# Kernel tuning notes

Measured on AMD Instinct MI355X. Metric: run time of the kernel, lower is better.

The kernel has to match this reference:

```python
import jax, jax.numpy as jnp
import numpy as np

N_HEADS = 8
N_LANDMARKS = 64
NEWTON_ITERS = 6


def _iterative_inv(mat):
    # mat: [B,H,L,L]; Newton-Schulz approximate inverse, 6 iterations
    L = mat.shape[-1]
    fro = jnp.sqrt(jnp.sum(mat * mat, axis=(-2, -1), keepdims=True))
    fro = jnp.maximum(fro, 1e-6)
    z = jnp.swapaxes(mat, -2, -1) / (fro * fro)
    for _ in range(NEWTON_ITERS):
        z = 2.0 * z - z @ mat @ z
    return z


def setup_inputs() -> dict:
    key = jax.random.key(0)
    ks = jax.random.split(key, 5)
    B, N, C = 4, 8192, 512
    s = 1.0 / np.sqrt(C)
    return {
        "x": jax.random.normal(ks[0], (B, N, C), jnp.float32),
        "Wqkv": jax.random.normal(ks[1], (3 * C, C), jnp.float32) * s,
        "bqkv": jax.random.normal(ks[2], (3 * C,), jnp.float32) * 0.01,
        "Wproj": jax.random.normal(ks[3], (C, C), jnp.float32) * s,
        "bproj": jax.random.normal(ks[4], (C,), jnp.float32) * 0.01,
    }


def reference(x, Wqkv, bqkv, Wproj, bproj):
    B, N, C = x.shape
    H = N_HEADS
    hd = C // H
    scale = hd ** (-0.5)
    n_lm = N_LANDMARKS

    qkv = x @ Wqkv.T + bqkv                       # [B,N,3C]
    qkv = qkv.reshape(B, N, 3, H, hd).transpose(2, 0, 3, 1, 4)  # [3,B,H,N,hd]
    q, k, v = qkv[0], qkv[1], qkv[2]

    if N <= n_lm:
        attn = jax.nn.softmax(q @ jnp.swapaxes(k, -2, -1) * scale, axis=-1)
        out = attn @ v
    else:
        stride = max(N // n_lm, 1)
        lm_idx = jnp.arange(0, N, stride)[:n_lm]
        q_lm = q[:, :, lm_idx]                    # [B,H,L,hd]
        k_lm = k[:, :, lm_idx]
        kernel_1 = jax.nn.softmax(q @ jnp.swapaxes(k_lm, -2, -1) * scale, axis=-1)   # [B,H,N,L]
        kernel_2 = jax.nn.softmax(q_lm @ jnp.swapaxes(k_lm, -2, -1) * scale, axis=-1)  # [B,H,L,L]
        kernel_3 = jax.nn.softmax(q_lm @ jnp.swapaxes(k, -2, -1) * scale, axis=-1)   # [B,H,L,N]
        kernel_2_inv = _iterative_inv(kernel_2)
        out = kernel_1 @ (kernel_2_inv @ (kernel_3 @ v))  # [B,H,N,hd]

    out = jnp.swapaxes(out, 1, 2).reshape(B, N, C)
    return out @ Wproj.T + bproj
```

## Files before the change

### kernel.cpp

```cpp
#include <hip/hip_runtime.h>

typedef unsigned short u16;
typedef unsigned int u32;

typedef __bf16 v8bf __attribute__((ext_vector_type(8)));
typedef float v4f __attribute__((ext_vector_type(4)));
typedef u16 v8u __attribute__((ext_vector_type(8)));

#define N_TOK 8192
#define CDIM 512
#define HEADS 8
#define HD 64
#define LM 64
#define LSTRIDE 128
#define BHN 32
#define NCHUNK 32
#define CHUNK 256
#define SCALE 0.125f

__device__ __forceinline__ float b2f(u16 u) { return __uint_as_float(((u32)u) << 16); }
__device__ __forceinline__ u16 f2bf(float f) {
  u32 u = __float_as_uint(f);
  u += 0x7fffu + ((u >> 16) & 1u);
  return (u16)(u >> 16);
}
__device__ __forceinline__ u32 pk2bf(float a, float b) {
  return (u32)f2bf(a) | ((u32)f2bf(b) << 16);
}

__device__ __forceinline__ void gl_lds16(const u16* g, u16* l) {
  __builtin_amdgcn_global_load_lds(
      (const __attribute__((address_space(1))) u32*)g,
      (__attribute__((address_space(3))) u32*)l, 16, 0, 0);
}

__device__ __forceinline__ void wr_hl(u16* __restrict__ h, u16* __restrict__ l,
                                      int row, int col, float v) {
  u16 hi = f2bf(v);
  u16 lo = f2bf(v - b2f(hi));
  int a = row * 64 + (((col >> 3) ^ (row & 7)) << 3) + (col & 7);
  h[a] = hi;
  l[a] = lo;
}

__global__ __launch_bounds__(256) void cast_bf16(const float* __restrict__ src,
                                                 u16* __restrict__ dst, int n8) {
  int i = blockIdx.x * 256 + threadIdx.x;
  if (i >= n8) return;
  const float4* s = (const float4*)src;
  float4 a = s[(size_t)i * 2], b = s[(size_t)i * 2 + 1];
  uint4 o;
  o.x = (u32)f2bf(a.x) | ((u32)f2bf(a.y) << 16);
  o.y = (u32)f2bf(a.z) | ((u32)f2bf(a.w) << 16);
  o.z = (u32)f2bf(b.x) | ((u32)f2bf(b.y) << 16);
  o.w = (u32)f2bf(b.z) | ((u32)f2bf(b.w) << 16);
  *(uint4*)(dst + (size_t)i * 8) = o;
}

__global__ __launch_bounds__(256) void cast_w2(const float* __restrict__ wa,
                                               const float* __restrict__ wb,
                                               u16* __restrict__ da,
                                               u16* __restrict__ db) {
  int i = blockIdx.x * 256 + threadIdx.x;
  const float* src;
  u16* dst;
  int j;
  if (i < 98304) { src = wa; dst = da; j = i; }
  else           { src = wb; dst = db; j = i - 98304; }
  const float4* s = (const float4*)src;
  float4 a = s[(size_t)j * 2], b = s[(size_t)j * 2 + 1];
  uint4 o;
  o.x = (u32)f2bf(a.x) | ((u32)f2bf(a.y) << 16);
  o.y = (u32)f2bf(a.z) | ((u32)f2bf(a.w) << 16);
  o.z = (u32)f2bf(b.x) | ((u32)f2bf(b.y) << 16);
  o.w = (u32)f2bf(b.z) | ((u32)f2bf(b.w) << 16);
  *(uint4*)(dst + (size_t)j * 8) = o;
}

template <int MODE>
__global__ __launch_bounds__(256) void gemm_bt(const u16* __restrict__ A,
                                               const u16* __restrict__ Bm,
                                               const float* __restrict__ bias,
                                               u16* __restrict__ qo,
                                               u16* __restrict__ ko,
                                               u16* __restrict__ vo,
                                               float* __restrict__ outp) {
  __shared__ __align__(16) u16 As[128 * 32];
  __shared__ __align__(16) u16 Bs[128 * 32];
  const int K = 512;
  const int m0 = blockIdx.x * 128;
  const int n0 = blockIdx.y * 128;
  const int t = threadIdx.x;
  const int lane = t & 63, w = t >> 6;
  const int wm = w >> 1, wn = w & 1;
  const int quad = lane >> 4, lrow = lane & 15;

  v4f acc[4][4];
#pragma unroll
  for (int i = 0; i < 4; ++i)
#pragma unroll
    for (int j = 0; j < 4; ++j)
#pragma unroll
      for (int r = 0; r < 4; ++r) acc[i][j][r] = 0.f;

  for (int kt = 0; kt < K; kt += 32) {
    __syncthreads();
#pragma unroll
    for (int p = 0; p < 2; ++p) {
      int ci = p * 256 + t;
      int r = ci >> 2, s = ci & 3;
      int cs = (s ^ (r >> 1)) & 3;
      gl_lds16(A + (size_t)(m0 + r) * K + kt + cs * 8, &As[ci * 8]);
      gl_lds16(Bm + (size_t)(n0 + r) * K + kt + cs * 8, &Bs[ci * 8]);
    }
    __syncthreads();
    v8bf af[4], bf[4];
#pragma unroll
    for (int ti = 0; ti < 4; ++ti) {
      int row = wm * 64 + ti * 16 + lrow;
      af[ti] = *(const v8bf*)&As[row * 32 + ((quad ^ (row >> 1)) & 3) * 8];
    }
#pragma unroll
    for (int tj = 0; tj < 4; ++tj) {
      int row = wn * 64 + tj * 16 + lrow;
      bf[tj] = *(const v8bf*)&Bs[row * 32 + ((quad ^ (row >> 1)) & 3) * 8];
    }
#pragma unroll
    for (int ti = 0; ti < 4; ++ti)
#pragma unroll
      for (int tj = 0; tj < 4; ++tj)
        acc[ti][tj] = __builtin_amdgcn_mfma_f32_16x16x32_bf16(af[ti], bf[tj], acc[ti][tj], 0, 0, 0);
  }

#pragma unroll
  for (int ti = 0; ti < 4; ++ti) {
#pragma unroll
    for (int tj = 0; tj < 4; ++tj) {
      int gn = n0 + wn * 64 + tj * 16 + lrow;
      float bv = bias[gn];
#pragma unroll
      for (int r = 0; r < 4; ++r) {
        int gm = m0 + wm * 64 + ti * 16 + quad * 4 + r;
        float val = acc[ti][tj][r] + bv;
        if (MODE == 0) {
          int tt = gn >> 9;
          int h = (gn >> 6) & 7;
          int d = gn & 63;
          int b = gm >> 13;
          int n = gm & 8191;
          size_t di = ((size_t)(b * HEADS + h) * N_TOK + n) * HD + d;
          u16* dst = (tt == 0) ? qo : (tt == 1) ? ko : vo;
          dst[di] = f2bf(val);
        } else {
          outp[(size_t)gm * CDIM + gn] = val;
        }
      }
    }
  }
}

__global__ __launch_bounds__(256) void fpart(const u16* __restrict__ qb,
                                             const u16* __restrict__ kb,
                                             const u16* __restrict__ vb,
                                             float* __restrict__ Fp,
                                             float* __restrict__ Mc,
                                             float* __restrict__ Sc) {
  __shared__ __align__(16) char smem[4 * 64 * 40 * 2 * 2];
  __shared__ float msh[4][64], ssh[4][64];
  const int jc = blockIdx.x, bh = blockIdx.y;
  const int t = threadIdx.x;
  const int lane = t & 63, w = t >> 6;
  const int col = lane & 15, quad = lane >> 4;
  const int jq = lane & 7, dh = lane >> 3;

  u16* Pw = (u16*)smem + w * (64 * 40);
  u16* vT = (u16*)smem + 4 * (64 * 40) + w * (64 * 40);
  float* Fbuf = (float*)smem;

  v8bf qf[4][2];
#pragma unroll
  for (int it = 0; it < 4; ++it)
#pragma unroll
    for (int kh = 0; kh < 2; ++kh)
      qf[it][kh] = *(const v8bf*)(qb + ((size_t)bh * N_TOK + (size_t)(it * 16 + col) * LSTRIDE) * HD + kh * 32 + quad * 8);

  float mw[4], sw[4];
  v4f facc[4][4];
#pragma unroll
  for (int it = 0; it < 4; ++it) { mw[it] = -3.0e38f; sw[it] = 0.f; }
#pragma unroll
  for (int dt = 0; dt < 4; ++dt)
#pragma unroll
    for (int it = 0; it < 4; ++it)
#pragma unroll
      for (int r = 0; r < 4; ++r) facc[dt][it][r] = 0.f;

  const size_t kv0 = (size_t)bh * N_TOK + jc * CHUNK + w * 64;

  v8bf kf[2][2];
  v8u vr[4];
#pragma unroll
  for (int jt = 0; jt < 2; ++jt)
#pragma unroll
    for (int kh = 0; kh < 2; ++kh)
      kf[jt][kh] = *(const v8bf*)(kb + (kv0 + jt * 16 + col) * HD + kh * 32 + quad * 8);
#pragma unroll
  for (int e = 0; e < 4; ++e)
    vr[e] = *(const v8u*)(vb + (kv0 + jq * 4 + e) * HD + dh * 8);

#pragma unroll
  for (int st = 0; st < 2; ++st) {
#pragma unroll
    for (int e = 0; e < 8; ++e) {
      uint2 pk;
      pk.x = (u32)vr[0][e] | ((u32)vr[1][e] << 16);
      pk.y = (u32)vr[2][e] | ((u32)vr[3][e] << 16);
      *(uint2*)&vT[(dh * 8 + e) * 40 + jq * 4] = pk;
    }

    v8bf kfn[2][2];
    v8u vrn[4];
    if (st < 1) {
      const size_t bn = kv0 + 32;
#pragma unroll
      for (int jt = 0; jt < 2; ++jt)
#pragma unroll
        for (int kh = 0; kh < 2; ++kh)
          kfn[jt][kh] = *(const v8bf*)(kb + (bn + jt * 16 + col) * HD + kh * 32 + quad * 8);
    }

    v4f sacc[2][4];
#pragma unroll
    for (int jt = 0; jt < 2; ++jt)
#pragma unroll
      for (int it = 0; it < 4; ++it) {
#pragma unroll
        for (int r = 0; r < 4; ++r) sacc[jt][it][r] = 0.f;
#pragma unroll
        for (int kh = 0; kh < 2; ++kh)
          sacc[jt][it] = __builtin_amdgcn_mfma_f32_16x16x32_bf16(kf[jt][kh], qf[it][kh], sacc[jt][it], 0, 0, 0);
      }

    if (st < 1) {
      const size_t bn = kv0 + 32;
#pragma unroll
      for (int e = 0; e < 4; ++e)
        vrn[e] = *(const v8u*)(vb + (bn + jq * 4 + e) * HD + dh * 8);
    }

#pragma unroll
    for (int it = 0; it < 4; ++it) {
      float mloc = -3.0e38f;
#pragma unroll
      for (int jt = 0; jt < 2; ++jt)
#pragma unroll
        for (int r = 0; r < 4; ++r) {
          float s = sacc[jt][it][r] * SCALE;
          sacc[jt][it][r] = s;
          mloc = fmaxf(mloc, s);
        }
      mloc = fmaxf(mloc, __shfl_xor(mloc, 16));
      mloc = fmaxf(mloc, __shfl_xor(mloc, 32));
      float mnew = fmaxf(mw[it], mloc);
      float alpha = __expf(mw[it] - mnew);
      mw[it] = mnew;
      float rs = 0.f;
#pragma unroll
      for (int jt = 0; jt < 2; ++jt)
#pragma unroll
        for (int r = 0; r < 4; ++r) {
          float p = __expf(sacc[jt][it][r] - mnew);
          sacc[jt][it][r] = p;
          rs += p;
        }
      rs += __shfl_xor(rs, 16);
      rs += __shfl_xor(rs, 32);
      sw[it] = sw[it] * alpha + rs;
#pragma unroll
      for (int jt = 0; jt < 2; ++jt) {
        uint2 pk;
        pk.x = pk2bf(sacc[jt][it][0], sacc[jt][it][1]);
        pk.y = pk2bf(sacc[jt][it][2], sacc[jt][it][3]);
        *(uint2*)&Pw[(it * 16 + col) * 40 + jt * 16 + quad * 4] = pk;
      }
#pragma unroll
      for (int dt = 0; dt < 4; ++dt)
#pragma unroll
        for (int r = 0; r < 4; ++r) facc[dt][it][r] *= alpha;
    }

    v8bf vfr[4], pfr[4];
#pragma unroll
    for (int dt = 0; dt < 4; ++dt)
      vfr[dt] = *(const v8bf*)&vT[(dt * 16 + col) * 40 + quad * 8];
#pragma unroll
    for (int it = 0; it < 4; ++it)
      pfr[it] = *(const v8bf*)&Pw[(it * 16 + col) * 40 + quad * 8];
#pragma unroll
    for (int dt = 0; dt < 4; ++dt)
#pragma unroll
      for (int it = 0; it < 4; ++it)
        facc[dt][it] = __builtin_amdgcn_mfma_f32_16x16x32_bf16(vfr[dt], pfr[it], facc[dt][it], 0, 0, 0);

    if (st < 1) {
#pragma unroll
      for (int jt = 0; jt < 2; ++jt)
#pragma unroll
        for (int kh = 0; kh < 2; ++kh)
          kf[jt][kh] = kfn[jt][kh];
#pragma unroll
      for (int e = 0; e < 4; ++e) vr[e] = vrn[e];
    }
  }

  if (quad == 0) {
#pragma unroll
    for (int it = 0; it < 4; ++it) {
      msh[w][it * 16 + col] = mw[it];
      ssh[w][it * 16 + col] = sw[it];
    }
  }
  __syncthreads();

  const size_t cb = (size_t)(bh * NCHUNK + jc) * 64;
  float scl[4];
#pragma unroll
  for (int it = 0; it < 4; ++it) {
    int i = it * 16 + col;
    float m0 = msh[0][i], m1 = msh[1][i], m2 = msh[2][i], m3 = msh[3][i];
    float M = fmaxf(fmaxf(m0, m1), fmaxf(m2, m3));
    float e0 = __expf(m0 - M), e1 = __expf(m1 - M);
    float e2 = __expf(m2 - M), e3 = __expf(m3 - M);
    float Stot = e0 * ssh[0][i] + e1 * ssh[1][i] + e2 * ssh[2][i] + e3 * ssh[3][i];
    scl[it] = (w == 0) ? e0 : (w == 1) ? e1 : (w == 2) ? e2 : e3;
    if (w == 0 && quad == 0) {
      Mc[cb + i] = M;
      Sc[cb + i] = Stot;
    }
  }

  for (int wv = 0; wv < 4; ++wv) {
    if (w == wv) {
#pragma unroll
      for (int it = 0; it < 4; ++it)
#pragma unroll
        for (int dt = 0; dt < 4; ++dt) {
          float* dst = &Fbuf[(it * 16 + col) * 76 + dt * 16 + quad * 4];
          float4 v;
          v.x = facc[dt][it][0] * scl[it];
          v.y = facc[dt][it][1] * scl[it];
          v.z = facc[dt][it][2] * scl[it];
          v.w = facc[dt][it][3] * scl[it];
          if (wv == 0) {
            *(float4*)dst = v;
          } else {
            float4 o = *(float4*)dst;
            o.x += v.x; o.y += v.y; o.z += v.z; o.w += v.w;
            *(float4*)dst = o;
          }
        }
    }
    __syncthreads();
  }

  size_t base = (size_t)(bh * NCHUNK + jc) * 4096;
#pragma unroll
  for (int p = 0; p < 16; ++p) {
    int idx = p * 256 + t;
    Fp[base + idx] = Fbuf[(idx >> 6) * 76 + (idx & 63)];
  }
}

__device__ __forceinline__ void mm_hl(const u16* __restrict__ Ah,
                                      const u16* __restrict__ Al,
                                      const u16* __restrict__ Bh,
                                      const u16* __restrict__ Bl,
                                      int Ra, int quad, int lrow, v4f out[4]) {
  v8bf ah[2], al[2];
#pragma unroll
  for (int kk = 0; kk < 2; ++kk) {
    int c8 = (((kk * 4 + quad) ^ (Ra & 7)) * 8);
    ah[kk] = *(const v8bf*)&Ah[Ra * 64 + c8];
    al[kk] = *(const v8bf*)&Al[Ra * 64 + c8];
  }
#pragma unroll
  for (int nt = 0; nt < 4; ++nt) {
    int Rb = nt * 16 + lrow;
#pragma unroll
    for (int kk = 0; kk < 2; ++kk) {
      int c8 = (((kk * 4 + quad) ^ (Rb & 7)) * 8);
      v8bf bh = *(const v8bf*)&Bh[Rb * 64 + c8];
      v8bf bl = *(const v8bf*)&Bl[Rb * 64 + c8];
      out[nt] = __builtin_amdgcn_mfma_f32_16x16x32_bf16(ah[kk], bh, out[nt], 0, 0, 0);
      out[nt] = __builtin_amdgcn_mfma_f32_16x16x32_bf16(ah[kk], bl, out[nt], 0, 0, 0);
      out[nt] = __builtin_amdgcn_mfma_f32_16x16x32_bf16(al[kk], bh, out[nt], 0, 0, 0);
    }
  }
}

__global__ __launch_bounds__(256) void newton_t(const u16* __restrict__ qb,
                                                const u16* __restrict__ kb,
                                                const float* __restrict__ Fp,
                                                const float* __restrict__ Mc,
                                                const float* __restrict__ Sc,
                                                u16* __restrict__ Tt) {
  __shared__ float Sf[4096];
  __shared__ float red[4];
  __shared__ __align__(16) u16 mTh[4096], mTl[4096];
  __shared__ __align__(16) u16 zh_[4096], zl_[4096];
  __shared__ __align__(16) u16 zTh[4096], zTl[4096];
  __shared__ __align__(16) u16 wh_[4096], wl_[4096];
  const int bh = blockIdx.x;
  const int t = threadIdx.x, lane = t & 63, w = t >> 6;
  const int quad = lane >> 4, lrow = lane & 15;
  const int Ra = w * 16 + lrow;
  const int Rd = w * 16 + quad * 4;

  {
    v8bf qf[2], kf[4][2];
#pragma unroll
    for (int kk = 0; kk < 2; ++kk)
      qf[kk] = *(const v8bf*)(qb + ((size_t)bh * N_TOK + (size_t)Ra * LSTRIDE) * HD + kk * 32 + quad * 8);
#pragma unroll
    for (int nt = 0; nt < 4; ++nt)
#pragma unroll
      for (int kk = 0; kk < 2; ++kk)
        kf[nt][kk] = *(const v8bf*)(kb + ((size_t)bh * N_TOK + (size_t)(nt * 16 + lrow) * LSTRIDE) * HD + kk * 32 + quad * 8);
    v4f sa[4];
#pragma unroll
    for (int nt = 0; nt < 4; ++nt) {
#pragma unroll
      for (int r = 0; r < 4; ++r) sa[nt][r] = 0.f;
#pragma unroll
      for (int kk = 0; kk < 2; ++kk)
        sa[nt] = __builtin_amdgcn_mfma_f32_16x16x32_bf16(qf[kk], kf[nt][kk], sa[nt], 0, 0, 0);
    }
#pragma unroll
    for (int nt = 0; nt < 4; ++nt)
#pragma unroll
      for (int r = 0; r < 4; ++r)
        Sf[(Rd + r) * 64 + nt * 16 + lrow] = sa[nt][r] * SCALE;
  }
  __syncthreads();

  for (int rr = 0; rr < 16; ++rr) {
    int i = w * 16 + rr;
    float vv = Sf[i * 64 + lane];
    float m = vv;
#pragma unroll
    for (int off = 32; off; off >>= 1) m = fmaxf(m, __shfl_xor(m, off));
    float e = expf(vv - m);
    float s = e;
#pragma unroll
    for (int off = 32; off; off >>= 1) s += __shfl_xor(s, off);
    Sf[i * 64 + lane] = e / s;
  }
  __syncthreads();

  float loc = 0.f;
#pragma unroll
  for (int p = 0; p < 16; ++p) {
    float v = Sf[p * 256 + t];
    loc += v * v;
  }
#pragma unroll
  for (int off = 32; off; off >>= 1) loc += __shfl_xor(loc, off);
  if (lane == 0) red[w] = loc;
  __syncthreads();
  float fro = fmaxf(sqrtf(red[0] + red[1] + red[2] + red[3]), 1e-6f);
  float inv = 1.0f / (fro * fro);

  for (int p = 0; p < 16; ++p) {
    int idx = p * 256 + t;
    int r = idx >> 6, c = idx & 63;
    float Mrc = Sf[r * 64 + c];
    float Mcr = Sf[c * 64 + r];
    wr_hl(mTh, mTl, r, c, Mcr);
    wr_hl(zh_, zl_, r, c, Mcr * inv);
    wr_hl(zTh, zTl, r, c, Mrc * inv);
  }
  float zr[4][4];
#pragma unroll
  for (int nt = 0; nt < 4; ++nt)
#pragma unroll
    for (int r = 0; r < 4; ++r)
      zr[nt][r] = Sf[(nt * 16 + lrow) * 64 + Rd + r] * inv;
  __syncthreads();

  for (int it = 0; it < 6; ++it) {
    v4f aw[4];
#pragma unroll
    for (int nt = 0; nt < 4; ++nt)
#pragma unroll
      for (int r = 0; r < 4; ++r) aw[nt][r] = 0.f;
    mm_hl(zh_, zl_, mTh, mTl, Ra, quad, lrow, aw);
#pragma unroll
    for (int nt = 0; nt < 4; ++nt)
#pragma unroll
      for (int r = 0; r < 4; ++r)
        wr_hl(wh_, wl_, Rd + r, nt * 16 + lrow, aw[nt][r]);
    __syncthreads();

    v4f ap[4];
#pragma unroll
    for (int nt = 0; nt < 4; ++nt)
#pragma unroll
      for (int r = 0; r < 4; ++r) ap[nt][r] = 0.f;
    mm_hl(wh_, wl_, zTh, zTl, Ra, quad, lrow, ap);
    float znr[4][4];
#pragma unroll
    for (int nt = 0; nt < 4; ++nt)
#pragma unroll
      for (int r = 0; r < 4; ++r)
        znr[nt][r] = 2.f * zr[nt][r] - ap[nt][r];
    __syncthreads();

#pragma unroll
    for (int nt = 0; nt < 4; ++nt)
#pragma unroll
      for (int r = 0; r < 4; ++r) {
        zr[nt][r] = znr[nt][r];
        wr_hl(zh_, zl_, Rd + r, nt * 16 + lrow, znr[nt][r]);
        wr_hl(zTh, zTl, nt * 16 + lrow, Rd + r, znr[nt][r]);
      }
    __syncthreads();
  }

  if (t < 64) {
    float M = -3.0e38f;
#pragma unroll
    for (int jc = 0; jc < NCHUNK; ++jc)
      M = fmaxf(M, Mc[(bh * NCHUNK + jc) * 64 + t]);
    float S = 0.f;
#pragma unroll
    for (int jc = 0; jc < NCHUNK; ++jc)
      S += expf(Mc[(bh * NCHUNK + jc) * 64 + t] - M) * Sc[(bh * NCHUNK + jc) * 64 + t];
    float invS = 1.0f / S;
#pragma unroll
    for (int jc = 0; jc < NCHUNK; ++jc)
      Sf[jc * 64 + t] = expf(Mc[(bh * NCHUNK + jc) * 64 + t] - M) * invS;
  }
  __syncthreads();

  for (int p = 0; p < 16; ++p) {
    int idx = p * 256 + t;
    int i = idx >> 6, d = idx & 63;
    float sum = 0.f;
#pragma unroll
    for (int jc = 0; jc < NCHUNK; ++jc)
      sum += Sf[jc * 64 + i] * Fp[(size_t)(bh * NCHUNK + jc) * 4096 + idx];
    wr_hl(wh_, wl_, d, i, sum);
  }
  __syncthreads();

  v4f at[4];
#pragma unroll
  for (int nt = 0; nt < 4; ++nt)
#pragma unroll
    for (int r = 0; r < 4; ++r) at[nt][r] = 0.f;
  mm_hl(zh_, zl_, wh_, wl_, Ra, quad, lrow, at);
#pragma unroll
  for (int nt = 0; nt < 4; ++nt)
#pragma unroll
    for (int r = 0; r < 4; ++r)
      Tt[(size_t)bh * 4096 + (size_t)(nt * 16 + lrow) * 64 + (Rd + r)] = f2bf(at[nt][r]);
}

__global__ __launch_bounds__(256) void attn_out_k(const u16* __restrict__ qb,
                                                  const u16* __restrict__ kb,
                                                  const u16* __restrict__ Tt,
                                                  u16* __restrict__ ao) {
  __shared__ __align__(16) u16 Pl[4][1024];
  const int bh = blockIdx.y;
  const int b = bh >> 3, h = bh & 7;
  const int t = threadIdx.x;
  const int lane = t & 63, w = t >> 6;
  const int col = lane & 15, quad = lane >> 4;
  const int rot = (col & 7) * 8;

  v8bf kfr[4][2], tfr[4][2];
#pragma unroll
  for (int tj = 0; tj < 4; ++tj)
#pragma unroll
    for (int kh = 0; kh < 2; ++kh)
      kfr[tj][kh] = *(const v8bf*)(kb + ((size_t)bh * N_TOK + (size_t)(tj * 16 + col) * LSTRIDE) * HD + kh * 32 + quad * 8);
#pragma unroll
  for (int td = 0; td < 4; ++td)
#pragma unroll
    for (int jh = 0; jh < 2; ++jh)
      tfr[td][jh] = *(const v8bf*)(Tt + (size_t)bh * 4096 + (size_t)(td * 16 + col) * 64 + jh * 32 + quad * 8);

  u16* Pw = &Pl[w][0];

  for (int tile = 0; tile < 4; ++tile) {
    const int n0 = blockIdx.x * 256 + w * 64 + tile * 16;
    v8bf qf[2];
#pragma unroll
    for (int kh = 0; kh < 2; ++kh)
      qf[kh] = *(const v8bf*)(qb + ((size_t)bh * N_TOK + n0 + col) * HD + kh * 32 + quad * 8);

    v4f S[4];
#pragma unroll
    for (int tj = 0; tj < 4; ++tj) {
#pragma unroll
      for (int r = 0; r < 4; ++r) S[tj][r] = 0.f;
#pragma unroll
      for (int kh = 0; kh < 2; ++kh)
        S[tj] = __builtin_amdgcn_mfma_f32_16x16x32_bf16(kfr[tj][kh], qf[kh], S[tj], 0, 0, 0);
    }

    float mx = -3.0e38f;
#pragma unroll
    for (int tj = 0; tj < 4; ++tj)
#pragma unroll
      for (int r = 0; r < 4; ++r) {
        S[tj][r] *= SCALE;
        mx = fmaxf(mx, S[tj][r]);
      }
    mx = fmaxf(mx, __shfl_xor(mx, 16));
    mx = fmaxf(mx, __shfl_xor(mx, 32));
    float sum = 0.f;
#pragma unroll
    for (int tj = 0; tj < 4; ++tj)
#pragma unroll
      for (int r = 0; r < 4; ++r) {
        S[tj][r] = __expf(S[tj][r] - mx);
        sum += S[tj][r];
      }
    sum += __shfl_xor(sum, 16);
    sum += __shfl_xor(sum, 32);
    float inv = 1.0f / sum;

#pragma unroll
    for (int tj = 0; tj < 4; ++tj) {
      u32 lo = (u32)f2bf(S[tj][0] * inv) | ((u32)f2bf(S[tj][1] * inv) << 16);
      u32 hi = (u32)f2bf(S[tj][2] * inv) | ((u32)f2bf(S[tj][3] * inv) << 16);
      uint2 pk = {lo, hi};
      *(uint2*)&Pw[col * 64 + ((tj * 16 + quad * 4 + rot) & 63)] = pk;
    }
    v8bf pf[2];
#pragma unroll
    for (int jh = 0; jh < 2; ++jh)
      pf[jh] = *(const v8bf*)&Pw[col * 64 + ((jh * 32 + quad * 8 + rot) & 63)];

    v4f O[4];
#pragma unroll
    for (int td = 0; td < 4; ++td) {
#pragma unroll
      for (int r = 0; r < 4; ++r) O[td][r] = 0.f;
#pragma unroll
      for (int jh = 0; jh < 2; ++jh)
        O[td] = __builtin_amdgcn_mfma_f32_16x16x32_bf16(pf[jh], tfr[td][jh], O[td], 0, 0, 0);
    }
#pragma unroll
    for (int td = 0; td < 4; ++td)
#pragma unroll
      for (int r = 0; r < 4; ++r) {
        int n = n0 + quad * 4 + r;
        ao[((size_t)(b * N_TOK + n)) * CDIM + h * HD + td * 16 + col] = f2bf(O[td][r]);
      }
  }
}

__global__ void ws_too_small_sentinel(float* out) {
  if (threadIdx.x == 0 && blockIdx.x == 0) out[0] = 1.0f;
}

static constexpr size_t SZ_QKV = (size_t)BHN * N_TOK * HD * 2;
static constexpr size_t OFF_Q = 0;
static constexpr size_t OFF_K = OFF_Q + SZ_QKV;
static constexpr size_t OFF_V = OFF_K + SZ_QKV;
static constexpr size_t OFF_FP = OFF_V + SZ_QKV;
static constexpr size_t SZ_FP = (size_t)BHN * NCHUNK * 4096 * 4;
static constexpr size_t OFF_MC = OFF_FP + SZ_FP;
static constexpr size_t SZ_MS = (size_t)BHN * NCHUNK * 64 * 4;
static constexpr size_t OFF_SC = OFF_MC + SZ_MS;
static constexpr size_t OFF_T = OFF_SC + SZ_MS;
static constexpr size_t OFF_WQ = OFF_T + (size_t)BHN * 4096 * 2;
static constexpr size_t OFF_WP = OFF_WQ + (size_t)3 * CDIM * CDIM * 2;
static constexpr size_t OFF_END = OFF_WP + (size_t)CDIM * CDIM * 2;

extern "C" void kernel_launch(void* const* d_in, const int* in_sizes, int n_in,
                              void* d_out, int out_size, void* d_ws, size_t ws_size,
                              hipStream_t stream) {
  const float* x = (const float*)d_in[0];
  const float* Wqkv = (const float*)d_in[1];
  const float* bqkv = (const float*)d_in[2];
  const float* Wproj = (const float*)d_in[3];
  const float* bproj = (const float*)d_in[4];
  float* out = (float*)d_out;
  char* ws = (char*)d_ws;
  if (ws_size < OFF_END) {
    ws_too_small_sentinel<<<1, 64, 0, stream>>>(out);
    return;
  }

  u16* qb = (u16*)(ws + OFF_Q);
  u16* kb = (u16*)(ws + OFF_K);
  u16* vb = (u16*)(ws + OFF_V);
  float* Fp = (float*)(ws + OFF_FP);
  float* Mc = (float*)(ws + OFF_MC);
  float* Sc = (float*)(ws + OFF_SC);
  u16* Tt = (u16*)(ws + OFF_T);
  u16* Wqb = (u16*)(ws + OFF_WQ);
  u16* Wpb = (u16*)(ws + OFF_WP);
  u16* attn = (u16*)(ws + OFF_V);
  u16* xb = (u16*)d_out;

  cast_bf16<<<8192, 256, 0, stream>>>(x, xb, 2097152);
  cast_w2<<<512, 256, 0, stream>>>(Wqkv, Wproj, Wqb, Wpb);
  gemm_bt<0><<<dim3(256, 12), 256, 0, stream>>>(xb, Wqb, bqkv, qb, kb, vb, nullptr);
  fpart<<<dim3(NCHUNK, BHN), 256, 0, stream>>>(qb, kb, vb, Fp, Mc, Sc);
  newton_t<<<dim3(BHN), 256, 0, stream>>>(qb, kb, Fp, Mc, Sc, Tt);
  attn_out_k<<<dim3(32, BHN), 256, 0, stream>>>(qb, kb, Tt, attn);
  gemm_bt<1><<<dim3(256, 4), 256, 0, stream>>>(attn, Wpb, bproj, nullptr, nullptr, nullptr, out);
}
```

Baseline: 302.8 us.

## Overlap Newton-Schulz inverse with partial K/V reduction in one launch

```diff
diff --git a/kernel.cpp b/kernel.cpp
--- a/kernel.cpp
+++ b/kernel.cpp
@@ -159,218 +159,6 @@
   }
 }
 
-__global__ __launch_bounds__(256) void fpart(const u16* __restrict__ qb,
-                                             const u16* __restrict__ kb,
-                                             const u16* __restrict__ vb,
-                                             float* __restrict__ Fp,
-                                             float* __restrict__ Mc,
-                                             float* __restrict__ Sc) {
-  __shared__ __align__(16) char smem[4 * 64 * 40 * 2 * 2];
-  __shared__ float msh[4][64], ssh[4][64];
-  const int jc = blockIdx.x, bh = blockIdx.y;
-  const int t = threadIdx.x;
-  const int lane = t & 63, w = t >> 6;
-  const int col = lane & 15, quad = lane >> 4;
-  const int jq = lane & 7, dh = lane >> 3;
-
-  u16* Pw = (u16*)smem + w * (64 * 40);
-  u16* vT = (u16*)smem + 4 * (64 * 40) + w * (64 * 40);
-  float* Fbuf = (float*)smem;
-
-  v8bf qf[4][2];
-#pragma unroll
-  for (int it = 0; it < 4; ++it)
-#pragma unroll
-    for (int kh = 0; kh < 2; ++kh)
-      qf[it][kh] = *(const v8bf*)(qb + ((size_t)bh * N_TOK + (size_t)(it * 16 + col) * LSTRIDE) * HD + kh * 32 + quad * 8);
-
-  float mw[4], sw[4];
-  v4f facc[4][4];
-#pragma unroll
-  for (int it = 0; it < 4; ++it) { mw[it] = -3.0e38f; sw[it] = 0.f; }
-#pragma unroll
-  for (int dt = 0; dt < 4; ++dt)
-#pragma unroll
-    for (int it = 0; it < 4; ++it)
-#pragma unroll
-      for (int r = 0; r < 4; ++r) facc[dt][it][r] = 0.f;
-
-  const size_t kv0 = (size_t)bh * N_TOK + jc * CHUNK + w * 64;
-
-  v8bf kf[2][2];
-  v8u vr[4];
-#pragma unroll
-  for (int jt = 0; jt < 2; ++jt)
-#pragma unroll
-    for (int kh = 0; kh < 2; ++kh)
-      kf[jt][kh] = *(const v8bf*)(kb + (kv0 + jt * 16 + col) * HD + kh * 32 + quad * 8);
-#pragma unroll
-  for (int e = 0; e < 4; ++e)
-    vr[e] = *(const v8u*)(vb + (kv0 + jq * 4 + e) * HD + dh * 8);
-
-#pragma unroll
-  for (int st = 0; st < 2; ++st) {
-#pragma unroll
-    for (int e = 0; e < 8; ++e) {
-      uint2 pk;
-      pk.x = (u32)vr[0][e] | ((u32)vr[1][e] << 16);
-      pk.y = (u32)vr[2][e] | ((u32)vr[3][e] << 16);
-      *(uint2*)&vT[(dh * 8 + e) * 40 + jq * 4] = pk;
-    }
-
-    v8bf kfn[2][2];
-    v8u vrn[4];
-    if (st < 1) {
-      const size_t bn = kv0 + 32;
-#pragma unroll
-      for (int jt = 0; jt < 2; ++jt)
-#pragma unroll
-        for (int kh = 0; kh < 2; ++kh)
-          kfn[jt][kh] = *(const v8bf*)(kb + (bn + jt * 16 + col) * HD + kh * 32 + quad * 8);
-    }
-
-    v4f sacc[2][4];
-#pragma unroll
-    for (int jt = 0; jt < 2; ++jt)
-#pragma unroll
-      for (int it = 0; it < 4; ++it) {
-#pragma unroll
-        for (int r = 0; r < 4; ++r) sacc[jt][it][r] = 0.f;
-#pragma unroll
-        for (int kh = 0; kh < 2; ++kh)
-          sacc[jt][it] = __builtin_amdgcn_mfma_f32_16x16x32_bf16(kf[jt][kh], qf[it][kh], sacc[jt][it], 0, 0, 0);
-      }
-
-    if (st < 1) {
-      const size_t bn = kv0 + 32;
-#pragma unroll
-      for (int e = 0; e < 4; ++e)
-        vrn[e] = *(const v8u*)(vb + (bn + jq * 4 + e) * HD + dh * 8);
-    }
-
-#pragma unroll
-    for (int it = 0; it < 4; ++it) {
-      float mloc = -3.0e38f;
-#pragma unroll
-      for (int jt = 0; jt < 2; ++jt)
-#pragma unroll
-        for (int r = 0; r < 4; ++r) {
-          float s = sacc[jt][it][r] * SCALE;
-          sacc[jt][it][r] = s;
-          mloc = fmaxf(mloc, s);
-        }
-      mloc = fmaxf(mloc, __shfl_xor(mloc, 16));
-      mloc = fmaxf(mloc, __shfl_xor(mloc, 32));
-      float mnew = fmaxf(mw[it], mloc);
-      float alpha = __expf(mw[it] - mnew);
-      mw[it] = mnew;
-      float rs = 0.f;
-#pragma unroll
-      for (int jt = 0; jt < 2; ++jt)
-#pragma unroll
-        for (int r = 0; r < 4; ++r) {
-          float p = __expf(sacc[jt][it][r] - mnew);
-          sacc[jt][it][r] = p;
-          rs += p;
-        }
-      rs += __shfl_xor(rs, 16);
-      rs += __shfl_xor(rs, 32);
-      sw[it] = sw[it] * alpha + rs;
-#pragma unroll
-      for (int jt = 0; jt < 2; ++jt) {
-        uint2 pk;
-        pk.x = pk2bf(sacc[jt][it][0], sacc[jt][it][1]);
-        pk.y = pk2bf(sacc[jt][it][2], sacc[jt][it][3]);
-        *(uint2*)&Pw[(it * 16 + col) * 40 + jt * 16 + quad * 4] = pk;
-      }
-#pragma unroll
-      for (int dt = 0; dt < 4; ++dt)
-#pragma unroll
-        for (int r = 0; r < 4; ++r) facc[dt][it][r] *= alpha;
-    }
-
-    v8bf vfr[4], pfr[4];
-#pragma unroll
-    for (int dt = 0; dt < 4; ++dt)
-      vfr[dt] = *(const v8bf*)&vT[(dt * 16 + col) * 40 + quad * 8];
-#pragma unroll
-    for (int it = 0; it < 4; ++it)
-      pfr[it] = *(const v8bf*)&Pw[(it * 16 + col) * 40 + quad * 8];
-#pragma unroll
-    for (int dt = 0; dt < 4; ++dt)
-#pragma unroll
-      for (int it = 0; it < 4; ++it)
-        facc[dt][it] = __builtin_amdgcn_mfma_f32_16x16x32_bf16(vfr[dt], pfr[it], facc[dt][it], 0, 0, 0);
-
-    if (st < 1) {
-#pragma unroll
-      for (int jt = 0; jt < 2; ++jt)
-#pragma unroll
-        for (int kh = 0; kh < 2; ++kh)
-          kf[jt][kh] = kfn[jt][kh];
-#pragma unroll
-      for (int e = 0; e < 4; ++e) vr[e] = vrn[e];
-    }
-  }
-
-  if (quad == 0) {
-#pragma unroll
-    for (int it = 0; it < 4; ++it) {
-      msh[w][it * 16 + col] = mw[it];
-      ssh[w][it * 16 + col] = sw[it];
-    }
-  }
-  __syncthreads();
-
-  const size_t cb = (size_t)(bh * NCHUNK + jc) * 64;
-  float scl[4];
-#pragma unroll
-  for (int it = 0; it < 4; ++it) {
-    int i = it * 16 + col;
-    float m0 = msh[0][i], m1 = msh[1][i], m2 = msh[2][i], m3 = msh[3][i];
-    float M = fmaxf(fmaxf(m0, m1), fmaxf(m2, m3));
-    float e0 = __expf(m0 - M), e1 = __expf(m1 - M);
-    float e2 = __expf(m2 - M), e3 = __expf(m3 - M);
-    float Stot = e0 * ssh[0][i] + e1 * ssh[1][i] + e2 * ssh[2][i] + e3 * ssh[3][i];
-    scl[it] = (w == 0) ? e0 : (w == 1) ? e1 : (w == 2) ? e2 : e3;
-    if (w == 0 && quad == 0) {
-      Mc[cb + i] = M;
-      Sc[cb + i] = Stot;
-    }
-  }
-
-  for (int wv = 0; wv < 4; ++wv) {
-    if (w == wv) {
-#pragma unroll
-      for (int it = 0; it < 4; ++it)
-#pragma unroll
-        for (int dt = 0; dt < 4; ++dt) {
-          float* dst = &Fbuf[(it * 16 + col) * 76 + dt * 16 + quad * 4];
-          float4 v;
-          v.x = facc[dt][it][0] * scl[it];
-          v.y = facc[dt][it][1] * scl[it];
-          v.z = facc[dt][it][2] * scl[it];
-          v.w = facc[dt][it][3] * scl[it];
-          if (wv == 0) {
-            *(float4*)dst = v;
-          } else {
-            float4 o = *(float4*)dst;
-            o.x += v.x; o.y += v.y; o.z += v.z; o.w += v.w;
-            *(float4*)dst = o;
-          }
-        }
-    }
-    __syncthreads();
-  }
-
-  size_t base = (size_t)(bh * NCHUNK + jc) * 4096;
-#pragma unroll
-  for (int p = 0; p < 16; ++p) {
-    int idx = p * 256 + t;
-    Fp[base + idx] = Fbuf[(idx >> 6) * 76 + (idx & 63)];
-  }
-}
-
 __device__ __forceinline__ void mm_hl(const u16* __restrict__ Ah,
                                       const u16* __restrict__ Al,
                                       const u16* __restrict__ Bh,
@@ -398,17 +186,360 @@
   }
 }
 
-__global__ __launch_bounds__(256) void newton_t(const u16* __restrict__ qb,
+__global__ __launch_bounds__(256) void fpart_nz(const u16* __restrict__ qb,
                                                 const u16* __restrict__ kb,
-                                                const float* __restrict__ Fp,
-                                                const float* __restrict__ Mc,
-                                                const float* __restrict__ Sc,
-                                                u16* __restrict__ Tt) {
-  __shared__ float Sf[4096];
+                                                const u16* __restrict__ vb,
+                                                float* __restrict__ Fp,
+                                                float* __restrict__ Mc,
+                                                float* __restrict__ Sc,
+                                                u16* __restrict__ Zb) {
+  __shared__ __align__(16) char smem[65536];
+  __shared__ float msh[4][64], ssh[4][64];
   __shared__ float red[4];
-  __shared__ __align__(16) u16 mTh[4096], mTl[4096];
+  const int jc = blockIdx.x, bh = blockIdx.y;
+  const int t = threadIdx.x;
+  const int lane = t & 63, w = t >> 6;
+  const int col = lane & 15, quad = lane >> 4;
+
+  if (jc < NCHUNK) {
+    const int jq = lane & 7, dh = lane >> 3;
+    u16* Pw = (u16*)smem + w * (64 * 40);
+    u16* vT = (u16*)smem + 4 * (64 * 40) + w * (64 * 40);
+    float* Fbuf = (float*)smem;
+
+    v8bf qf[4][2];
+#pragma unroll
+    for (int it = 0; it < 4; ++it)
+#pragma unroll
+      for (int kh = 0; kh < 2; ++kh)
+        qf[it][kh] = *(const v8bf*)(qb + ((size_t)bh * N_TOK + (size_t)(it * 16 + col) * LSTRIDE) * HD + kh * 32 + quad * 8);
+
+    float mw[4], sw[4];
+    v4f facc[4][4];
+#pragma unroll
+    for (int it = 0; it < 4; ++it) { mw[it] = -3.0e38f; sw[it] = 0.f; }
+#pragma unroll
+    for (int dt = 0; dt < 4; ++dt)
+#pragma unroll
+      for (int it = 0; it < 4; ++it)
+#pragma unroll
+        for (int r = 0; r < 4; ++r) facc[dt][it][r] = 0.f;
+
+    const size_t kv0 = (size_t)bh * N_TOK + jc * CHUNK + w * 64;
+
+    v8bf kf[2][2];
+    v8u vr[4];
+#pragma unroll
+    for (int jt = 0; jt < 2; ++jt)
+#pragma unroll
+      for (int kh = 0; kh < 2; ++kh)
+        kf[jt][kh] = *(const v8bf*)(kb + (kv0 + jt * 16 + col) * HD + kh * 32 + quad * 8);
+#pragma unroll
+    for (int e = 0; e < 4; ++e)
+      vr[e] = *(const v8u*)(vb + (kv0 + jq * 4 + e) * HD + dh * 8);
+
+#pragma unroll
+    for (int st = 0; st < 2; ++st) {
+#pragma unroll
+      for (int e = 0; e < 8; ++e) {
+        uint2 pk;
+        pk.x = (u32)vr[0][e] | ((u32)vr[1][e] << 16);
+        pk.y = (u32)vr[2][e] | ((u32)vr[3][e] << 16);
+        *(uint2*)&vT[(dh * 8 + e) * 40 + jq * 4] = pk;
+      }
+
+      v8bf kfn[2][2];
+      v8u vrn[4];
+      if (st < 1) {
+        const size_t bn = kv0 + 32;
+#pragma unroll
+        for (int jt = 0; jt < 2; ++jt)
+#pragma unroll
+          for (int kh = 0; kh < 2; ++kh)
+            kfn[jt][kh] = *(const v8bf*)(kb + (bn + jt * 16 + col) * HD + kh * 32 + quad * 8);
+      }
+
+      v4f sacc[2][4];
+#pragma unroll
+      for (int jt = 0; jt < 2; ++jt)
+#pragma unroll
+        for (int it = 0; it < 4; ++it) {
+#pragma unroll
+          for (int r = 0; r < 4; ++r) sacc[jt][it][r] = 0.f;
+#pragma unroll
+          for (int kh = 0; kh < 2; ++kh)
+            sacc[jt][it] = __builtin_amdgcn_mfma_f32_16x16x32_bf16(kf[jt][kh], qf[it][kh], sacc[jt][it], 0, 0, 0);
+        }
+
+      if (st < 1) {
+        const size_t bn = kv0 + 32;
+#pragma unroll
+        for (int e = 0; e < 4; ++e)
+          vrn[e] = *(const v8u*)(vb + (bn + jq * 4 + e) * HD + dh * 8);
+      }
+
+#pragma unroll
+      for (int it = 0; it < 4; ++it) {
+        float mloc = -3.0e38f;
+#pragma unroll
+        for (int jt = 0; jt < 2; ++jt)
+#pragma unroll
+          for (int r = 0; r < 4; ++r) {
+            float s = sacc[jt][it][r] * SCALE;
+            sacc[jt][it][r] = s;
+            mloc = fmaxf(mloc, s);
+          }
+        mloc = fmaxf(mloc, __shfl_xor(mloc, 16));
+        mloc = fmaxf(mloc, __shfl_xor(mloc, 32));
+        float mnew = fmaxf(mw[it], mloc);
+        float alpha = __expf(mw[it] - mnew);
+        mw[it] = mnew;
+        float rs = 0.f;
+#pragma unroll
+        for (int jt = 0; jt < 2; ++jt)
+#pragma unroll
+          for (int r = 0; r < 4; ++r) {
+            float p = __expf(sacc[jt][it][r] - mnew);
+            sacc[jt][it][r] = p;
+            rs += p;
+          }
+        rs += __shfl_xor(rs, 16);
+        rs += __shfl_xor(rs, 32);
+        sw[it] = sw[it] * alpha + rs;
+#pragma unroll
+        for (int jt = 0; jt < 2; ++jt) {
+          uint2 pk;
+          pk.x = pk2bf(sacc[jt][it][0], sacc[jt][it][1]);
+          pk.y = pk2bf(sacc[jt][it][2], sacc[jt][it][3]);
+          *(uint2*)&Pw[(it * 16 + col) * 40 + jt * 16 + quad * 4] = pk;
+        }
+#pragma unroll
+        for (int dt = 0; dt < 4; ++dt)
+#pragma unroll
+          for (int r = 0; r < 4; ++r) facc[dt][it][r] *= alpha;
+      }
+
+      v8bf vfr[4], pfr[4];
+#pragma unroll
+      for (int dt = 0; dt < 4; ++dt)
+        vfr[dt] = *(const v8bf*)&vT[(dt * 16 + col) * 40 + quad * 8];
+#pragma unroll
+      for (int it = 0; it < 4; ++it)
+        pfr[it] = *(const v8bf*)&Pw[(it * 16 + col) * 40 + quad * 8];
+#pragma unroll
+      for (int dt = 0; dt < 4; ++dt)
+#pragma unroll
+        for (int it = 0; it < 4; ++it)
+          facc[dt][it] = __builtin_amdgcn_mfma_f32_16x16x32_bf16(vfr[dt], pfr[it], facc[dt][it], 0, 0, 0);
+
+      if (st < 1) {
+#pragma unroll
+        for (int jt = 0; jt < 2; ++jt)
+#pragma unroll
+          for (int kh = 0; kh < 2; ++kh)
+            kf[jt][kh] = kfn[jt][kh];
+#pragma unroll
+        for (int e = 0; e < 4; ++e) vr[e] = vrn[e];
+      }
+    }
+
+    if (quad == 0) {
+#pragma unroll
+      for (int it = 0; it < 4; ++it) {
+        msh[w][it * 16 + col] = mw[it];
+        ssh[w][it * 16 + col] = sw[it];
+      }
+    }
+    __syncthreads();
+
+    const size_t cb = (size_t)(bh * NCHUNK + jc) * 64;
+    float scl[4];
+#pragma unroll
+    for (int it = 0; it < 4; ++it) {
+      int i = it * 16 + col;
+      float m0 = msh[0][i], m1 = msh[1][i], m2 = msh[2][i], m3 = msh[3][i];
+      float M = fmaxf(fmaxf(m0, m1), fmaxf(m2, m3));
+      float e0 = __expf(m0 - M), e1 = __expf(m1 - M);
+      float e2 = __expf(m2 - M), e3 = __expf(m3 - M);
+      float Stot = e0 * ssh[0][i] + e1 * ssh[1][i] + e2 * ssh[2][i] + e3 * ssh[3][i];
+      scl[it] = (w == 0) ? e0 : (w == 1) ? e1 : (w == 2) ? e2 : e3;
+      if (w == 0 && quad == 0) {
+        Mc[cb + i] = M;
+        Sc[cb + i] = Stot;
+      }
+    }
+
+    for (int wv = 0; wv < 4; ++wv) {
+      if (w == wv) {
+#pragma unroll
+        for (int it = 0; it < 4; ++it)
+#pragma unroll
+          for (int dt = 0; dt < 4; ++dt) {
+            float* dst = &Fbuf[(it * 16 + col) * 76 + dt * 16 + quad * 4];
+            float4 v;
+            v.x = facc[dt][it][0] * scl[it];
+            v.y = facc[dt][it][1] * scl[it];
+            v.z = facc[dt][it][2] * scl[it];
+            v.w = facc[dt][it][3] * scl[it];
+            if (wv == 0) {
+              *(float4*)dst = v;
+            } else {
+              float4 o = *(float4*)dst;
+              o.x += v.x; o.y += v.y; o.z += v.z; o.w += v.w;
+              *(float4*)dst = o;
+            }
+          }
+      }
+      __syncthreads();
+    }
+
+    size_t base = (size_t)(bh * NCHUNK + jc) * 4096;
+#pragma unroll
+    for (int p = 0; p < 16; ++p) {
+      int idx = p * 256 + t;
+      Fp[base + idx] = Fbuf[(idx >> 6) * 76 + (idx & 63)];
+    }
+  } else {
+    float* Sf = (float*)smem;
+    u16* wh_ = (u16*)smem;
+    u16* wl_ = (u16*)(smem + 8192);
+    u16* mTh = (u16*)(smem + 16384);
+    u16* mTl = (u16*)(smem + 24576);
+    u16* zh_ = (u16*)(smem + 32768);
+    u16* zl_ = (u16*)(smem + 40960);
+    u16* zTh = (u16*)(smem + 49152);
+    u16* zTl = (u16*)(smem + 57344);
+    const int lrow = lane & 15;
+    const int Ra = w * 16 + lrow;
+    const int Rd = w * 16 + quad * 4;
+
+    {
+      v8bf qf[2], kf[4][2];
+#pragma unroll
+      for (int kk = 0; kk < 2; ++kk)
+        qf[kk] = *(const v8bf*)(qb + ((size_t)bh * N_TOK + (size_t)Ra * LSTRIDE) * HD + kk * 32 + quad * 8);
+#pragma unroll
+      for (int nt = 0; nt < 4; ++nt)
+#pragma unroll
+        for (int kk = 0; kk < 2; ++kk)
+          kf[nt][kk] = *(const v8bf*)(kb + ((size_t)bh * N_TOK + (size_t)(nt * 16 + lrow) * LSTRIDE) * HD + kk * 32 + quad * 8);
+      v4f sa[4];
+#pragma unroll
+      for (int nt = 0; nt < 4; ++nt) {
+#pragma unroll
+        for (int r = 0; r < 4; ++r) sa[nt][r] = 0.f;
+#pragma unroll
+        for (int kk = 0; kk < 2; ++kk)
+          sa[nt] = __builtin_amdgcn_mfma_f32_16x16x32_bf16(qf[kk], kf[nt][kk], sa[nt], 0, 0, 0);
+      }
+#pragma unroll
+      for (int nt = 0; nt < 4; ++nt)
+#pragma unroll
+        for (int r = 0; r < 4; ++r)
+          Sf[(Rd + r) * 64 + nt * 16 + lrow] = sa[nt][r] * SCALE;
+    }
+    __syncthreads();
+
+    for (int rr = 0; rr < 16; ++rr) {
+      int i = w * 16 + rr;
+      float vv = Sf[i * 64 + lane];
+      float m = vv;
+#pragma unroll
+      for (int off = 32; off; off >>= 1) m = fmaxf(m, __shfl_xor(m, off));
+      float e = expf(vv - m);
+      float s = e;
+#pragma unroll
+      for (int off = 32; off; off >>= 1) s += __shfl_xor(s, off);
+      Sf[i * 64 + lane] = e / s;
+    }
+    __syncthreads();
+
+    float loc = 0.f;
+#pragma unroll
+    for (int p = 0; p < 16; ++p) {
+      float v = Sf[p * 256 + t];
+      loc += v * v;
+    }
+#pragma unroll
+    for (int off = 32; off; off >>= 1) loc += __shfl_xor(loc, off);
+    if (lane == 0) red[w] = loc;
+    __syncthreads();
+    float fro = fmaxf(sqrtf(red[0] + red[1] + red[2] + red[3]), 1e-6f);
+    float inv = 1.0f / (fro * fro);
+
+    for (int p = 0; p < 16; ++p) {
+      int idx = p * 256 + t;
+      int r = idx >> 6, c = idx & 63;
+      float Mrc = Sf[r * 64 + c];
+      float Mcr = Sf[c * 64 + r];
+      wr_hl(mTh, mTl, r, c, Mcr);
+      wr_hl(zh_, zl_, r, c, Mcr * inv);
+      wr_hl(zTh, zTl, r, c, Mrc * inv);
+    }
+    float zr[4][4];
+#pragma unroll
+    for (int nt = 0; nt < 4; ++nt)
+#pragma unroll
+      for (int r = 0; r < 4; ++r)
+        zr[nt][r] = Sf[(nt * 16 + lrow) * 64 + Rd + r] * inv;
+    __syncthreads();
+
+    for (int it = 0; it < 6; ++it) {
+      v4f aw[4];
+#pragma unroll
+      for (int nt = 0; nt < 4; ++nt)
+#pragma unroll
+        for (int r = 0; r < 4; ++r) aw[nt][r] = 0.f;
+      mm_hl(zh_, zl_, mTh, mTl, Ra, quad, lrow, aw);
+#pragma unroll
+      for (int nt = 0; nt < 4; ++nt)
+#pragma unroll
+        for (int r = 0; r < 4; ++r)
+          wr_hl(wh_, wl_, Rd + r, nt * 16 + lrow, aw[nt][r]);
+      __syncthreads();
+
+      v4f ap[4];
+#pragma unroll
+      for (int nt = 0; nt < 4; ++nt)
+#pragma unroll
+        for (int r = 0; r < 4; ++r) ap[nt][r] = 0.f;
+      mm_hl(wh_, wl_, zTh, zTl, Ra, quad, lrow, ap);
+      float znr[4][4];
+#pragma unroll
+      for (int nt = 0; nt < 4; ++nt)
+#pragma unroll
+        for (int r = 0; r < 4; ++r)
+          znr[nt][r] = 2.f * zr[nt][r] - ap[nt][r];
+      __syncthreads();
+
+#pragma unroll
+      for (int nt = 0; nt < 4; ++nt)
+#pragma unroll
+        for (int r = 0; r < 4; ++r) {
+          zr[nt][r] = znr[nt][r];
+          wr_hl(zh_, zl_, Rd + r, nt * 16 + lrow, znr[nt][r]);
+          wr_hl(zTh, zTl, nt * 16 + lrow, Rd + r, znr[nt][r]);
+        }
+      __syncthreads();
+    }
+
+    uint4* zdst = (uint4*)(Zb + (size_t)bh * 8192);
+    const uint4* s1 = (const uint4*)zh_;
+    const uint4* s2 = (const uint4*)zl_;
+    zdst[t] = s1[t];
+    zdst[256 + t] = s1[256 + t];
+    zdst[512 + t] = s2[t];
+    zdst[768 + t] = s2[256 + t];
+  }
+}
+
+__global__ __launch_bounds__(256) void newton_combine(const float* __restrict__ Fp,
+                                                      const float* __restrict__ Mc,
+                                                      const float* __restrict__ Sc,
+                                                      const u16* __restrict__ Zb,
+                                                      u16* __restrict__ Tt) {
+  __shared__ float wsh[NCHUNK * 64];
   __shared__ __align__(16) u16 zh_[4096], zl_[4096];
-  __shared__ __align__(16) u16 zTh[4096], zTl[4096];
   __shared__ __align__(16) u16 wh_[4096], wl_[4096];
   const int bh = blockIdx.x;
   const int t = threadIdx.x, lane = t & 63, w = t >> 6;
@@ -417,113 +548,13 @@
   const int Rd = w * 16 + quad * 4;
 
   {
-    v8bf qf[2], kf[4][2];
-#pragma unroll
-    for (int kk = 0; kk < 2; ++kk)
-      qf[kk] = *(const v8bf*)(qb + ((size_t)bh * N_TOK + (size_t)Ra * LSTRIDE) * HD + kk * 32 + quad * 8);
-#pragma unroll
-    for (int nt = 0; nt < 4; ++nt)
-#pragma unroll
-      for (int kk = 0; kk < 2; ++kk)
-        kf[nt][kk] = *(const v8bf*)(kb + ((size_t)bh * N_TOK + (size_t)(nt * 16 + lrow) * LSTRIDE) * HD + kk * 32 + quad * 8);
-    v4f sa[4];
-#pragma unroll
-    for (int nt = 0; nt < 4; ++nt) {
-#pragma unroll
-      for (int r = 0; r < 4; ++r) sa[nt][r] = 0.f;
-#pragma unroll
-      for (int kk = 0; kk < 2; ++kk)
-        sa[nt] = __builtin_amdgcn_mfma_f32_16x16x32_bf16(qf[kk], kf[nt][kk], sa[nt], 0, 0, 0);
-    }
-#pragma unroll
-    for (int nt = 0; nt < 4; ++nt)
-#pragma unroll
-      for (int r = 0; r < 4; ++r)
-        Sf[(Rd + r) * 64 + nt * 16 + lrow] = sa[nt][r] * SCALE;
-  }
-  __syncthreads();
-
-  for (int rr = 0; rr < 16; ++rr) {
-    int i = w * 16 + rr;
-    float vv = Sf[i * 64 + lane];
-    float m = vv;
-#pragma unroll
-    for (int off = 32; off; off >>= 1) m = fmaxf(m, __shfl_xor(m, off));
-    float e = expf(vv - m);
-    float s = e;
-#pragma unroll
-    for (int off = 32; off; off >>= 1) s += __shfl_xor(s, off);
-    Sf[i * 64 + lane] = e / s;
-  }
-  __syncthreads();
-
-  float loc = 0.f;
-#pragma unroll
-  for (int p = 0; p < 16; ++p) {
-    float v = Sf[p * 256 + t];
-    loc += v * v;
-  }
-#pragma unroll
-  for (int off = 32; off; off >>= 1) loc += __shfl_xor(loc, off);
-  if (lane == 0) red[w] = loc;
-  __syncthreads();
-  float fro = fmaxf(sqrtf(red[0] + red[1] + red[2] + red[3]), 1e-6f);
-  float inv = 1.0f / (fro * fro);
-
-  for (int p = 0; p < 16; ++p) {
-    int idx = p * 256 + t;
-    int r = idx >> 6, c = idx & 63;
-    float Mrc = Sf[r * 64 + c];
-    float Mcr = Sf[c * 64 + r];
-    wr_hl(mTh, mTl, r, c, Mcr);
-    wr_hl(zh_, zl_, r, c, Mcr * inv);
-    wr_hl(zTh, zTl, r, c, Mrc * inv);
-  }
-  float zr[4][4];
-#pragma unroll
-  for (int nt = 0; nt < 4; ++nt)
-#pragma unroll
-    for (int r = 0; r < 4; ++r)
-      zr[nt][r] = Sf[(nt * 16 + lrow) * 64 + Rd + r] * inv;
-  __syncthreads();
-
-  for (int it = 0; it < 6; ++it) {
-    v4f aw[4];
-#pragma unroll
-    for (int nt = 0; nt < 4; ++nt)
-#pragma unroll
-      for (int r = 0; r < 4; ++r) aw[nt][r] = 0.f;
-    mm_hl(zh_, zl_, mTh, mTl, Ra, quad, lrow, aw);
-#pragma unroll
-    for (int nt = 0; nt < 4; ++nt)
-#pragma unroll
-      for (int r = 0; r < 4; ++r)
-        wr_hl(wh_, wl_, Rd + r, nt * 16 + lrow, aw[nt][r]);
-    __syncthreads();
-
-    v4f ap[4];
-#pragma unroll
-    for (int nt = 0; nt < 4; ++nt)
-#pragma unroll
-      for (int r = 0; r < 4; ++r) ap[nt][r] = 0.f;
-    mm_hl(wh_, wl_, zTh, zTl, Ra, quad, lrow, ap);
-    float znr[4][4];
-#pragma unroll
-    for (int nt = 0; nt < 4; ++nt)
-#pragma unroll
-      for (int r = 0; r < 4; ++r)
-        znr[nt][r] = 2.f * zr[nt][r] - ap[nt][r];
-    __syncthreads();
-
-#pragma unroll
-    for (int nt = 0; nt < 4; ++nt)
-#pragma unroll
-      for (int r = 0; r < 4; ++r) {
-        zr[nt][r] = znr[nt][r];
-        wr_hl(zh_, zl_, Rd + r, nt * 16 + lrow, znr[nt][r]);
-        wr_hl(zTh, zTl, nt * 16 + lrow, Rd + r, znr[nt][r]);
-      }
-    __syncthreads();
+    const uint4* zsrc = (const uint4*)(Zb + (size_t)bh * 8192);
+    uint4* d1 = (uint4*)zh_;
+    uint4* d2 = (uint4*)zl_;
+    d1[t] = zsrc[t];
+    d1[256 + t] = zsrc[256 + t];
+    d2[t] = zsrc[512 + t];
+    d2[256 + t] = zsrc[768 + t];
   }
 
   if (t < 64) {
@@ -538,7 +569,7 @@
     float invS = 1.0f / S;
 #pragma unroll
     for (int jc = 0; jc < NCHUNK; ++jc)
-      Sf[jc * 64 + t] = expf(Mc[(bh * NCHUNK + jc) * 64 + t] - M) * invS;
+      wsh[jc * 64 + t] = expf(Mc[(bh * NCHUNK + jc) * 64 + t] - M) * invS;
   }
   __syncthreads();
 
@@ -548,7 +579,7 @@
     float sum = 0.f;
 #pragma unroll
     for (int jc = 0; jc < NCHUNK; ++jc)
-      sum += Sf[jc * 64 + i] * Fp[(size_t)(bh * NCHUNK + jc) * 4096 + idx];
+      sum += wsh[jc * 64 + i] * Fp[(size_t)(bh * NCHUNK + jc) * 4096 + idx];
     wr_hl(wh_, wl_, d, i, sum);
   }
   __syncthreads();
@@ -678,7 +709,8 @@
 static constexpr size_t OFF_T = OFF_SC + SZ_MS;
 static constexpr size_t OFF_WQ = OFF_T + (size_t)BHN * 4096 * 2;
 static constexpr size_t OFF_WP = OFF_WQ + (size_t)3 * CDIM * CDIM * 2;
-static constexpr size_t OFF_END = OFF_WP + (size_t)CDIM * CDIM * 2;
+static constexpr size_t OFF_ZB = OFF_WP + (size_t)CDIM * CDIM * 2;
+static constexpr size_t OFF_END = OFF_ZB + (size_t)BHN * 8192 * 2;
 
 extern "C" void kernel_launch(void* const* d_in, const int* in_sizes, int n_in,
                               void* d_out, int out_size, void* d_ws, size_t ws_size,
@@ -704,14 +736,15 @@
   u16* Tt = (u16*)(ws + OFF_T);
   u16* Wqb = (u16*)(ws + OFF_WQ);
   u16* Wpb = (u16*)(ws + OFF_WP);
+  u16* Zb = (u16*)(ws + OFF_ZB);
   u16* attn = (u16*)(ws + OFF_V);
   u16* xb = (u16*)d_out;
 
   cast_bf16<<<8192, 256, 0, stream>>>(x, xb, 2097152);
   cast_w2<<<512, 256, 0, stream>>>(Wqkv, Wproj, Wqb, Wpb);
   gemm_bt<0><<<dim3(256, 12), 256, 0, stream>>>(xb, Wqb, bqkv, qb, kb, vb, nullptr);
-  fpart<<<dim3(NCHUNK, BHN), 256, 0, stream>>>(qb, kb, vb, Fp, Mc, Sc);
-  newton_t<<<dim3(BHN), 256, 0, stream>>>(qb, kb, Fp, Mc, Sc, Tt);
+  fpart_nz<<<dim3(NCHUNK + 1, BHN), 256, 0, stream>>>(qb, kb, vb, Fp, Mc, Sc, Zb);
+  newton_combine<<<BHN, 256, 0, stream>>>(Fp, Mc, Sc, Zb, Tt);
   attn_out_k<<<dim3(32, BHN), 256, 0, stream>>>(qb, kb, Tt, attn);
   gemm_bt<1><<<dim3(256, 4), 256, 0, stream>>>(attn, Wpb, bproj, nullptr, nullptr, nullptr, out);
 }
```

Result: slower. 350.5 us (+15.8%).
